# Performance work log

Hardware: AMD Instinct MI355X
Metric: run time of the kernel (lower is better)

The kernel has to match this reference:

```python
import jax, jax.numpy as jnp
import numpy as np

EPS = 1e-8


def setup_inputs() -> dict:
    key = jax.random.key(0)
    k1, k2, k3, k4 = jax.random.split(key, 4)
    B, N, M, C = 512, 512, 128, 1024
    addr = M + 6  # read head: k(M) + beta(1) + g(1) + s(3) + gamma(1)
    controller_out = jax.random.normal(k1, (B, C), dtype=jnp.float32)
    prev_w = jax.random.uniform(k2, (B, N), dtype=jnp.float32)
    prev_w = prev_w / prev_w.sum(axis=1, keepdims=True)  # valid weighting
    memory_state = jax.random.normal(k3, (B, N, M), dtype=jnp.float32)
    W_fc = jax.random.normal(k4, (C, addr), dtype=jnp.float32) * 0.02
    b_fc = jnp.zeros((addr,), dtype=jnp.float32)
    return {"controller_out": controller_out, "prev_w": prev_w,
            "memory_state": memory_state, "W_fc": W_fc, "b_fc": b_fc}


def reference(controller_out, prev_w, memory_state, W_fc, b_fc):
    M = memory_state.shape[2]
    out = controller_out @ W_fc + b_fc  # [B, M+6]
    k = out[:, :M]                                   # key
    beta = jax.nn.softplus(out[:, M:M + 1])          # key strength
    g = jax.nn.sigmoid(out[:, M + 1:M + 2])          # interpolation gate
    s = jax.nn.softmax(out[:, M + 2:M + 5], axis=1)  # 3-tap shift weights
    gamma = 1.0 + jax.nn.softplus(out[:, M + 5:M + 6])

    # Content addressing (Eq. 5-6): cosine similarity + sharpened softmax
    norm_k = jnp.linalg.norm(k, axis=1, keepdims=True) + EPS      # [B,1]
    norm_mem = jnp.linalg.norm(memory_state, axis=2) + EPS        # [B,N]
    sim = jnp.einsum('bnm,bm->bn', memory_state, k) / (norm_k * norm_mem)
    w_c = jax.nn.softmax(beta * sim, axis=1)

    # Interpolation (Eq. 7)
    w_g = g * w_c + (1.0 - g) * prev_w

    # Circular 3-tap shift (Eq. 8): vectorized roll instead of per-slot loop
    w_s = (s[:, 0:1] * jnp.roll(w_g, 1, axis=1)
           + s[:, 1:2] * w_g
           + s[:, 2:3] * jnp.roll(w_g, -1, axis=1))

    # Sharpening (Eq. 9)
    w_pow = w_s ** gamma
    w = w_pow / (w_pow.sum(axis=1, keepdims=True) + EPS)

    # Read vector (read head)
    read_vec = jnp.einsum('bn,bnm->bm', w, memory_state)
    return (read_vec, w)
```

## Files before the change

### kernel.cpp

```cpp
#include <hip/hip_runtime.h>
#include <math.h>

#define BB   512
#define NN   512
#define MM   128
#define CC   1024
#define ADDR 134
#define EPSF 1e-8f

#define KEEP(x) asm volatile("" : "+v"(x))

__device__ __forceinline__ float softplus_f(float x) {
    return fmaxf(x, 0.0f) + log1pf(expf(-fabsf(x)));
}

__global__ __launch_bounds__(1024, 4) void ntm_head_kernel(
    const float* __restrict__ co,
    const float* __restrict__ prev_w,
    const float* __restrict__ mem,
    const float* __restrict__ W_fc,
    const float* __restrict__ b_fc,
    float* __restrict__ out_rv,
    float* __restrict__ out_w)
{
    __shared__ __align__(16) float s_co[CC];
    __shared__ __align__(16) float s_k[MM];
    __shared__ float s_extra[8];
    __shared__ __align__(16) float s_bsim[NN];
    __shared__ float s_wg[NN];
    __shared__ float s_w[NN];
    __shared__ __align__(16) float s_part[32 * MM];
    __shared__ float s_red[16];
    __shared__ float s_params[8];

    const int t = threadIdx.x;
    const int b = blockIdx.x;
    const int gi = t >> 5;
    const int l  = t & 31;
    const float4* memb = (const float4*)(mem + (size_t)b * NN * MM);

    s_co[t] = co[(size_t)b * CC + t];
    float pw = (t < NN) ? prev_w[(size_t)b * NN + t] : 0.0f;

    float4 p[16];
    #pragma unroll
    for (int jj = 0; jj < 16; ++jj)
        p[jj] = memb[(size_t)gi * 32 + l + (size_t)jj * 1024];

    __syncthreads();

    {
        const int o    = t & (MM - 1);
        const int part = t >> 7;
        const float* Wp = W_fc + o;
        float a0 = 0.f, a1 = 0.f, a2 = 0.f, a3 = 0.f;
        const int c0 = part * (CC / 8);
        for (int c = c0; c < c0 + CC / 8; c += 4) {
            float4 cv = *(const float4*)(s_co + c);
            a0 = fmaf(cv.x, Wp[(size_t)(c + 0) * ADDR], a0);
            a1 = fmaf(cv.y, Wp[(size_t)(c + 1) * ADDR], a1);
            a2 = fmaf(cv.z, Wp[(size_t)(c + 2) * ADDR], a2);
            a3 = fmaf(cv.w, Wp[(size_t)(c + 3) * ADDR], a3);
        }
        s_part[part * MM + o] = (a0 + a1) + (a2 + a3);

        const int wv = t >> 6;
        if (wv < 6) {
            const int ll = t & 63;
            const int oe = MM + wv;
            const float* We = W_fc + oe;
            float e = 0.f;
            for (int c = ll; c < CC; c += 64)
                e = fmaf(s_co[c], We[(size_t)c * ADDR], e);
            #pragma unroll
            for (int off = 32; off >= 1; off >>= 1) e += __shfl_xor(e, off, 64);
            if (ll == 0) s_extra[wv] = e + b_fc[oe];
        }
    }

    #pragma unroll
    for (int jj = 0; jj < 16; ++jj) {
        KEEP(p[jj].x); KEEP(p[jj].y); KEEP(p[jj].z); KEEP(p[jj].w);
    }

    __syncthreads();

    if (t < MM) {
        float r = b_fc[t];
        #pragma unroll
        for (int q = 0; q < 8; ++q) r += s_part[q * MM + t];
        s_k[t] = r;
        float v = r * r;
        #pragma unroll
        for (int off = 32; off >= 1; off >>= 1) v += __shfl_xor(v, off, 64);
        if ((t & 63) == 0) s_red[t >> 6] = v;
    }
    __syncthreads();
    if (t == 0) {
        float ks = s_red[0] + s_red[1];
        float norm_k = sqrtf(ks) + EPSF;
        float beta = softplus_f(s_extra[0]);
        float g = 1.0f / (1.0f + expf(-s_extra[1]));
        float e0 = s_extra[2], e1 = s_extra[3], e2 = s_extra[4];
        float mx = fmaxf(e0, fmaxf(e1, e2));
        float x0 = expf(e0 - mx), x1 = expf(e1 - mx), x2 = expf(e2 - mx);
        float inv = 1.0f / (x0 + x1 + x2);
        s_params[0] = beta / norm_k;
        s_params[1] = g;
        s_params[2] = x0 * inv;
        s_params[3] = x1 * inv;
        s_params[4] = x2 * inv;
        s_params[5] = 1.0f + softplus_f(s_extra[5]);
    }
    __syncthreads();

    const float bnk = s_params[0];
    const float4 kv = ((const float4*)s_k)[l];

    #pragma unroll
    for (int j = 0; j < 16; j += 4) {
        float d0 = p[j  ].x*kv.x + p[j  ].y*kv.y + p[j  ].z*kv.z + p[j  ].w*kv.w;
        float d1 = p[j+1].x*kv.x + p[j+1].y*kv.y + p[j+1].z*kv.z + p[j+1].w*kv.w;
        float d2 = p[j+2].x*kv.x + p[j+2].y*kv.y + p[j+2].z*kv.z + p[j+2].w*kv.w;
        float d3 = p[j+3].x*kv.x + p[j+3].y*kv.y + p[j+3].z*kv.z + p[j+3].w*kv.w;
        float q0 = p[j  ].x*p[j  ].x + p[j  ].y*p[j  ].y + p[j  ].z*p[j  ].z + p[j  ].w*p[j  ].w;
        float q1 = p[j+1].x*p[j+1].x + p[j+1].y*p[j+1].y + p[j+1].z*p[j+1].z + p[j+1].w*p[j+1].w;
        float q2 = p[j+2].x*p[j+2].x + p[j+2].y*p[j+2].y + p[j+2].z*p[j+2].z + p[j+2].w*p[j+2].w;
        float q3 = p[j+3].x*p[j+3].x + p[j+3].y*p[j+3].y + p[j+3].z*p[j+3].z + p[j+3].w*p[j+3].w;

        d0 += __shfl_xor(d0, 16, 64); q0 += __shfl_xor(q0, 16, 64);
        d1 += __shfl_xor(d1, 16, 64); q1 += __shfl_xor(q1, 16, 64);
        d2 += __shfl_xor(d2, 16, 64); q2 += __shfl_xor(q2, 16, 64);
        d3 += __shfl_xor(d3, 16, 64); q3 += __shfl_xor(q3, 16, 64);
        float W0 = (l & 16) ? q0 : d0;
        float W1 = (l & 16) ? q1 : d1;
        float W2 = (l & 16) ? q2 : d2;
        float W3 = (l & 16) ? q3 : d3;
        W0 += __shfl_xor(W0, 8, 64); W1 += __shfl_xor(W1, 8, 64);
        W2 += __shfl_xor(W2, 8, 64); W3 += __shfl_xor(W3, 8, 64);
        float X0 = (l & 8) ? W1 : W0;
        float X1 = (l & 8) ? W3 : W2;
        X0 += __shfl_xor(X0, 4, 64); X1 += __shfl_xor(X1, 4, 64);
        float Y = (l & 4) ? X1 : X0;
        Y += __shfl_xor(Y, 2, 64);
        Y += __shfl_xor(Y, 1, 64);
        float Q = __shfl_xor(Y, 16, 64);
        if (l < 16 && (l & 3) == 0) {
            int jj = j + ((l & 4) >> 1) + ((l & 8) >> 3);
            s_bsim[gi + jj * 32] = bnk * Y / (sqrtf(Q) + EPSF);
        }
    }
    __syncthreads();

    float wp1 = 0.0f;
    {
        const float NEG = -3.0e38f;
        float b1 = (t < NN) ? s_bsim[t] : NEG;

        float m = b1;
        #pragma unroll
        for (int off = 32; off >= 1; off >>= 1) m = fmaxf(m, __shfl_xor(m, off, 64));
        if ((t & 63) == 0) s_red[t >> 6] = m;
        __syncthreads();
        float M8 = s_red[0];
        #pragma unroll
        for (int i = 1; i < 8; ++i) M8 = fmaxf(M8, s_red[i]);
        __syncthreads();

        float e1 = (t < NN) ? expf(b1 - M8) : 0.0f;
        float ls = e1;
        #pragma unroll
        for (int off = 32; off >= 1; off >>= 1) ls += __shfl_xor(ls, off, 64);
        if ((t & 63) == 0) s_red[t >> 6] = ls;
        __syncthreads();
        float S = s_red[0];
        #pragma unroll
        for (int i = 1; i < 8; ++i) S += s_red[i];
        __syncthreads();

        const float invS = 1.0f / S;
        const float g = s_params[1];
        float wg1 = fmaf(g, e1 * invS, (1.0f - g) * pw);
        if (t < NN) s_wg[t] = wg1;
        __syncthreads();

        const float sh0 = s_params[2], sh1 = s_params[3], sh2 = s_params[4];
        const float gamma = s_params[5];
        if (t < NN) {
            float ws1 = sh0 * s_wg[(t + NN - 1) & (NN - 1)]
                      + sh1 * wg1
                      + sh2 * s_wg[(t + 1) & (NN - 1)];
            wp1 = powf(ws1, gamma);
            s_w[t] = wp1;
        }
    }
    __syncthreads();

    {
        float4 acc = make_float4(0.f, 0.f, 0.f, 0.f);
        #pragma unroll
        for (int jj = 0; jj < 16; ++jj) {
            float w = s_w[gi + jj * 32];
            acc.x = fmaf(w, p[jj].x, acc.x);
            acc.y = fmaf(w, p[jj].y, acc.y);
            acc.z = fmaf(w, p[jj].z, acc.z);
            acc.w = fmaf(w, p[jj].w, acc.w);
        }

        float lz = wp1;
        #pragma unroll
        for (int off = 32; off >= 1; off >>= 1) lz += __shfl_xor(lz, off, 64);
        if ((t & 63) == 0) s_red[t >> 6] = lz;

        *((float4*)&s_part[gi * MM + l * 4]) = acc;
        __syncthreads();

        float Z = s_red[0];
        #pragma unroll
        for (int i = 1; i < 8; ++i) Z += s_red[i];
        const float invZ = 1.0f / (Z + EPSF);

        if (t < NN) out_w[(size_t)b * NN + t] = wp1 * invZ;

        if (t < 512) {
            const int h = t >> 7;
            const int o = t & (MM - 1);
            float r = 0.f;
            #pragma unroll
            for (int q = 0; q < 8; ++q) r += s_part[(h * 8 + q) * MM + o];
            s_bsim[h * MM + o] = r;
        }
        __syncthreads();
        if (t < MM) {
            float r = s_bsim[t] + s_bsim[MM + t] + s_bsim[2 * MM + t] + s_bsim[3 * MM + t];
            out_rv[(size_t)b * MM + t] = r * invZ;
        }
    }
}

extern "C" void kernel_launch(void* const* d_in, const int* in_sizes, int n_in,
                              void* d_out, int out_size, void* d_ws, size_t ws_size,
                              hipStream_t stream) {
    const float* co     = (const float*)d_in[0];
    const float* prev_w = (const float*)d_in[1];
    const float* mem    = (const float*)d_in[2];
    const float* W_fc   = (const float*)d_in[3];
    const float* b_fc   = (const float*)d_in[4];
    float* out = (float*)d_out;
    ntm_head_kernel<<<BB, 1024, 0, stream>>>(co, prev_w, mem, W_fc, b_fc,
                                             out, out + (size_t)BB * MM);
}
```

Before: 230.9 us.

## Split fused NTM head kernel into FC, similarity, and tail kernels

Replaces the single fused kernel, which held each batch's memory slice in registers, with three kernels. The first computes the FC projection for two batches per block so each W_fc load is shared, then writes the key scaled by beta/norm and the addressing parameters to workspace. The second spreads the cosine-similarity pass over four times as many smaller blocks. The third does the softmax, shift and sharpening and re-reads memory for the read vector. The aim is better parallelism and less register pressure, at the cost of reading the 134 MB memory tensor twice and adding launch and workspace traffic.

```diff
diff --git a/kernel.cpp b/kernel.cpp
--- a/kernel.cpp
+++ b/kernel.cpp
@@ -8,45 +8,31 @@
 #define ADDR 134
 #define EPSF 1e-8f
 
-#define KEEP(x) asm volatile("" : "+v"(x))
-
 __device__ __forceinline__ float softplus_f(float x) {
     return fmaxf(x, 0.0f) + log1pf(expf(-fabsf(x)));
 }
 
-__global__ __launch_bounds__(1024, 4) void ntm_head_kernel(
-    const float* __restrict__ co,
-    const float* __restrict__ prev_w,
-    const float* __restrict__ mem,
-    const float* __restrict__ W_fc,
-    const float* __restrict__ b_fc,
-    float* __restrict__ out_rv,
-    float* __restrict__ out_w)
+__global__ __launch_bounds__(512) void k1_fc(
+    const float* __restrict__ co, const float* __restrict__ W_fc,
+    const float* __restrict__ b_fc, float* __restrict__ ws_kk,
+    float* __restrict__ ws_par)
 {
-    __shared__ __align__(16) float s_co[CC];
-    __shared__ __align__(16) float s_k[MM];
-    __shared__ float s_extra[8];
-    __shared__ __align__(16) float s_bsim[NN];
-    __shared__ float s_wg[NN];
-    __shared__ float s_w[NN];
-    __shared__ __align__(16) float s_part[32 * MM];
-    __shared__ float s_red[16];
-    __shared__ float s_params[8];
-
-    const int t = threadIdx.x;
-    const int b = blockIdx.x;
-    const int gi = t >> 5;
-    const int l  = t & 31;
-    const float4* memb = (const float4*)(mem + (size_t)b * NN * MM);
-
-    s_co[t] = co[(size_t)b * CC + t];
-    float pw = (t < NN) ? prev_w[(size_t)b * NN + t] : 0.0f;
-
-    float4 p[16];
-    #pragma unroll
-    for (int jj = 0; jj < 16; ++jj)
-        p[jj] = memb[(size_t)gi * 32 + l + (size_t)jj * 1024];
-
+    __shared__ __align__(16) float s_co0[CC];
+    __shared__ __align__(16) float s_co1[CC];
+    __shared__ float s_part0[4 * MM];
+    __shared__ float s_part1[4 * MM];
+    __shared__ float s_extra[2][8];
+    __shared__ float s_red[2][2];
+    __shared__ float s_scale[2];
+
+    const int t  = threadIdx.x;
+    const int b0 = blockIdx.x;
+    const int b1 = blockIdx.x + 256;
+
+    s_co0[t]       = co[(size_t)b0 * CC + t];
+    s_co0[t + 512] = co[(size_t)b0 * CC + t + 512];
+    s_co1[t]       = co[(size_t)b1 * CC + t];
+    s_co1[t + 512] = co[(size_t)b1 * CC + t + 512];
     __syncthreads();
 
     {
@@ -54,79 +40,114 @@
         const int part = t >> 7;
         const float* Wp = W_fc + o;
         float a0 = 0.f, a1 = 0.f, a2 = 0.f, a3 = 0.f;
-        const int c0 = part * (CC / 8);
-        for (int c = c0; c < c0 + CC / 8; c += 4) {
-            float4 cv = *(const float4*)(s_co + c);
-            a0 = fmaf(cv.x, Wp[(size_t)(c + 0) * ADDR], a0);
-            a1 = fmaf(cv.y, Wp[(size_t)(c + 1) * ADDR], a1);
-            a2 = fmaf(cv.z, Wp[(size_t)(c + 2) * ADDR], a2);
-            a3 = fmaf(cv.w, Wp[(size_t)(c + 3) * ADDR], a3);
+        float d0 = 0.f, d1 = 0.f, d2 = 0.f, d3 = 0.f;
+        const int cc0 = part * 256;
+        for (int c = cc0; c < cc0 + 256; c += 4) {
+            float w0 = Wp[(size_t)(c + 0) * ADDR];
+            float w1 = Wp[(size_t)(c + 1) * ADDR];
+            float w2 = Wp[(size_t)(c + 2) * ADDR];
+            float w3 = Wp[(size_t)(c + 3) * ADDR];
+            float4 u = *(const float4*)(s_co0 + c);
+            float4 v = *(const float4*)(s_co1 + c);
+            a0 = fmaf(u.x, w0, a0); a1 = fmaf(u.y, w1, a1);
+            a2 = fmaf(u.z, w2, a2); a3 = fmaf(u.w, w3, a3);
+            d0 = fmaf(v.x, w0, d0); d1 = fmaf(v.y, w1, d1);
+            d2 = fmaf(v.z, w2, d2); d3 = fmaf(v.w, w3, d3);
         }
-        s_part[part * MM + o] = (a0 + a1) + (a2 + a3);
+        s_part0[part * MM + o] = (a0 + a1) + (a2 + a3);
+        s_part1[part * MM + o] = (d0 + d1) + (d2 + d3);
 
         const int wv = t >> 6;
         if (wv < 6) {
             const int ll = t & 63;
             const int oe = MM + wv;
             const float* We = W_fc + oe;
-            float e = 0.f;
-            for (int c = ll; c < CC; c += 64)
-                e = fmaf(s_co[c], We[(size_t)c * ADDR], e);
+            float e0 = 0.f, e1 = 0.f;
+            for (int c = ll; c < CC; c += 64) {
+                float w = We[(size_t)c * ADDR];
+                e0 = fmaf(s_co0[c], w, e0);
+                e1 = fmaf(s_co1[c], w, e1);
+            }
             #pragma unroll
-            for (int off = 32; off >= 1; off >>= 1) e += __shfl_xor(e, off, 64);
-            if (ll == 0) s_extra[wv] = e + b_fc[oe];
+            for (int off = 32; off >= 1; off >>= 1) {
+                e0 += __shfl_xor(e0, off, 64);
+                e1 += __shfl_xor(e1, off, 64);
+            }
+            if (ll == 0) {
+                s_extra[0][wv] = e0 + b_fc[oe];
+                s_extra[1][wv] = e1 + b_fc[oe];
+            }
         }
     }
-
-    #pragma unroll
-    for (int jj = 0; jj < 16; ++jj) {
-        KEEP(p[jj].x); KEEP(p[jj].y); KEEP(p[jj].z); KEEP(p[jj].w);
-    }
-
-    __syncthreads();
-
+    __syncthreads();
+
+    float k0 = 0.f, k1v = 0.f;
     if (t < MM) {
-        float r = b_fc[t];
+        float bias = b_fc[t];
+        k0  = bias + s_part0[t] + s_part0[MM + t] + s_part0[2 * MM + t] + s_part0[3 * MM + t];
+        k1v = bias + s_part1[t] + s_part1[MM + t] + s_part1[2 * MM + t] + s_part1[3 * MM + t];
+        float v0 = k0 * k0, v1 = k1v * k1v;
         #pragma unroll
-        for (int q = 0; q < 8; ++q) r += s_part[q * MM + t];
-        s_k[t] = r;
-        float v = r * r;
-        #pragma unroll
-        for (int off = 32; off >= 1; off >>= 1) v += __shfl_xor(v, off, 64);
-        if ((t & 63) == 0) s_red[t >> 6] = v;
-    }
-    __syncthreads();
-    if (t == 0) {
-        float ks = s_red[0] + s_red[1];
+        for (int off = 32; off >= 1; off >>= 1) {
+            v0 += __shfl_xor(v0, off, 64);
+            v1 += __shfl_xor(v1, off, 64);
+        }
+        if ((t & 63) == 0) { s_red[0][t >> 6] = v0; s_red[1][t >> 6] = v1; }
+    }
+    __syncthreads();
+    if (t < 2) {
+        const int bs = t;
+        const int bb = bs ? b1 : b0;
+        float ks = s_red[bs][0] + s_red[bs][1];
         float norm_k = sqrtf(ks) + EPSF;
-        float beta = softplus_f(s_extra[0]);
-        float g = 1.0f / (1.0f + expf(-s_extra[1]));
-        float e0 = s_extra[2], e1 = s_extra[3], e2 = s_extra[4];
+        float beta = softplus_f(s_extra[bs][0]);
+        float g = 1.0f / (1.0f + expf(-s_extra[bs][1]));
+        float e0 = s_extra[bs][2], e1 = s_extra[bs][3], e2 = s_extra[bs][4];
         float mx = fmaxf(e0, fmaxf(e1, e2));
         float x0 = expf(e0 - mx), x1 = expf(e1 - mx), x2 = expf(e2 - mx);
         float inv = 1.0f / (x0 + x1 + x2);
-        s_params[0] = beta / norm_k;
-        s_params[1] = g;
-        s_params[2] = x0 * inv;
-        s_params[3] = x1 * inv;
-        s_params[4] = x2 * inv;
-        s_params[5] = 1.0f + softplus_f(s_extra[5]);
-    }
-    __syncthreads();
-
-    const float bnk = s_params[0];
-    const float4 kv = ((const float4*)s_k)[l];
+        s_scale[bs] = beta / norm_k;
+        float* pp = ws_par + (size_t)bb * 8;
+        pp[0] = g;
+        pp[1] = x0 * inv; pp[2] = x1 * inv; pp[3] = x2 * inv;
+        pp[4] = 1.0f + softplus_f(s_extra[bs][5]);
+    }
+    __syncthreads();
+    if (t < MM) {
+        ws_kk[(size_t)b0 * MM + t] = k0  * s_scale[0];
+        ws_kk[(size_t)b1 * MM + t] = k1v * s_scale[1];
+    }
+}
+
+__global__ __launch_bounds__(256) void k2_sim(
+    const float* __restrict__ mem, const float* __restrict__ ws_kk,
+    float* __restrict__ ws_bsim)
+{
+    const int bb   = blockIdx.x;
+    const int b    = bb >> 2;
+    const int tile = bb & 3;
+    const int t = threadIdx.x;
+    const int g = t >> 5;
+    const int l = t & 31;
+    const float4* memb = (const float4*)(mem + (size_t)b * NN * MM) + (size_t)tile * 128 * 32;
+    const float4 kv = ((const float4*)(ws_kk + (size_t)b * MM))[l];
+    float* bs = ws_bsim + (size_t)b * NN + tile * 128;
 
     #pragma unroll
     for (int j = 0; j < 16; j += 4) {
-        float d0 = p[j  ].x*kv.x + p[j  ].y*kv.y + p[j  ].z*kv.z + p[j  ].w*kv.w;
-        float d1 = p[j+1].x*kv.x + p[j+1].y*kv.y + p[j+1].z*kv.z + p[j+1].w*kv.w;
-        float d2 = p[j+2].x*kv.x + p[j+2].y*kv.y + p[j+2].z*kv.z + p[j+2].w*kv.w;
-        float d3 = p[j+3].x*kv.x + p[j+3].y*kv.y + p[j+3].z*kv.z + p[j+3].w*kv.w;
-        float q0 = p[j  ].x*p[j  ].x + p[j  ].y*p[j  ].y + p[j  ].z*p[j  ].z + p[j  ].w*p[j  ].w;
-        float q1 = p[j+1].x*p[j+1].x + p[j+1].y*p[j+1].y + p[j+1].z*p[j+1].z + p[j+1].w*p[j+1].w;
-        float q2 = p[j+2].x*p[j+2].x + p[j+2].y*p[j+2].y + p[j+2].z*p[j+2].z + p[j+2].w*p[j+2].w;
-        float q3 = p[j+3].x*p[j+3].x + p[j+3].y*p[j+3].y + p[j+3].z*p[j+3].z + p[j+3].w*p[j+3].w;
+        float4 a0 = memb[(size_t)(g + (j + 0) * 8) * 32 + l];
+        float4 a1 = memb[(size_t)(g + (j + 1) * 8) * 32 + l];
+        float4 a2 = memb[(size_t)(g + (j + 2) * 8) * 32 + l];
+        float4 a3 = memb[(size_t)(g + (j + 3) * 8) * 32 + l];
+
+        float d0 = a0.x*kv.x + a0.y*kv.y + a0.z*kv.z + a0.w*kv.w;
+        float d1 = a1.x*kv.x + a1.y*kv.y + a1.z*kv.z + a1.w*kv.w;
+        float d2 = a2.x*kv.x + a2.y*kv.y + a2.z*kv.z + a2.w*kv.w;
+        float d3 = a3.x*kv.x + a3.y*kv.y + a3.z*kv.z + a3.w*kv.w;
+        float q0 = a0.x*a0.x + a0.y*a0.y + a0.z*a0.z + a0.w*a0.w;
+        float q1 = a1.x*a1.x + a1.y*a1.y + a1.z*a1.z + a1.w*a1.w;
+        float q2 = a2.x*a2.x + a2.y*a2.y + a2.z*a2.z + a2.w*a2.w;
+        float q3 = a3.x*a3.x + a3.y*a3.y + a3.z*a3.z + a3.w*a3.w;
 
         d0 += __shfl_xor(d0, 16, 64); q0 += __shfl_xor(q0, 16, 64);
         d1 += __shfl_xor(d1, 16, 64); q1 += __shfl_xor(q1, 16, 64);
@@ -147,94 +168,120 @@
         float Q = __shfl_xor(Y, 16, 64);
         if (l < 16 && (l & 3) == 0) {
             int jj = j + ((l & 4) >> 1) + ((l & 8) >> 3);
-            s_bsim[gi + jj * 32] = bnk * Y / (sqrtf(Q) + EPSF);
+            bs[g + jj * 8] = Y / (sqrtf(Q) + EPSF);
         }
     }
+}
+
+__global__ __launch_bounds__(1024) void k3_tail(
+    const float* __restrict__ prev_w, const float* __restrict__ mem,
+    const float* __restrict__ ws_bsim, const float* __restrict__ ws_par,
+    float* __restrict__ out_rv, float* __restrict__ out_w)
+{
+    __shared__ float s_wg[NN];
+    __shared__ float s_w[NN];
+    __shared__ __align__(16) float s_part[32 * MM];
+    __shared__ float s_scr[4 * MM];
+    __shared__ float s_red[16];
+
+    const int t = threadIdx.x;
+    const int b = blockIdx.x;
+    const int gi = t >> 5;
+    const int l  = t & 31;
+    const float4* memb = (const float4*)(mem + (size_t)b * NN * MM);
+
+    float pw = (t < NN) ? prev_w[(size_t)b * NN + t] : 0.0f;
+    const float NEG = -3.0e38f;
+    float b1 = (t < NN) ? ws_bsim[(size_t)b * NN + t] : NEG;
+    const float g     = ws_par[(size_t)b * 8 + 0];
+    const float sh0   = ws_par[(size_t)b * 8 + 1];
+    const float sh1   = ws_par[(size_t)b * 8 + 2];
+    const float sh2   = ws_par[(size_t)b * 8 + 3];
+    const float gamma = ws_par[(size_t)b * 8 + 4];
+
+    float m = b1;
+    #pragma unroll
+    for (int off = 32; off >= 1; off >>= 1) m = fmaxf(m, __shfl_xor(m, off, 64));
+    if ((t & 63) == 0) s_red[t >> 6] = m;
+    __syncthreads();
+    float M8 = s_red[0];
+    #pragma unroll
+    for (int i = 1; i < 8; ++i) M8 = fmaxf(M8, s_red[i]);
+    __syncthreads();
+
+    float e1 = (t < NN) ? expf(b1 - M8) : 0.0f;
+    float ls = e1;
+    #pragma unroll
+    for (int off = 32; off >= 1; off >>= 1) ls += __shfl_xor(ls, off, 64);
+    if ((t & 63) == 0) s_red[t >> 6] = ls;
+    __syncthreads();
+    float S = s_red[0];
+    #pragma unroll
+    for (int i = 1; i < 8; ++i) S += s_red[i];
+    __syncthreads();
+
+    const float invS = 1.0f / S;
+    float wg1 = fmaf(g, e1 * invS, (1.0f - g) * pw);
+    if (t < NN) s_wg[t] = wg1;
     __syncthreads();
 
     float wp1 = 0.0f;
-    {
-        const float NEG = -3.0e38f;
-        float b1 = (t < NN) ? s_bsim[t] : NEG;
-
-        float m = b1;
+    if (t < NN) {
+        float ws1 = sh0 * s_wg[(t + NN - 1) & (NN - 1)]
+                  + sh1 * wg1
+                  + sh2 * s_wg[(t + 1) & (NN - 1)];
+        wp1 = powf(ws1, gamma);
+        s_w[t] = wp1;
+    }
+    __syncthreads();
+
+    float4 acc = make_float4(0.f, 0.f, 0.f, 0.f);
+    for (int j = 0; j < 16; j += 4) {
+        float4 a0 = memb[(size_t)(gi + (j + 0) * 32) * 32 + l];
+        float4 a1 = memb[(size_t)(gi + (j + 1) * 32) * 32 + l];
+        float4 a2 = memb[(size_t)(gi + (j + 2) * 32) * 32 + l];
+        float4 a3 = memb[(size_t)(gi + (j + 3) * 32) * 32 + l];
+        float w0 = s_w[gi + (j + 0) * 32];
+        float w1 = s_w[gi + (j + 1) * 32];
+        float w2 = s_w[gi + (j + 2) * 32];
+        float w3 = s_w[gi + (j + 3) * 32];
+        acc.x = fmaf(w0, a0.x, acc.x); acc.y = fmaf(w0, a0.y, acc.y);
+        acc.z = fmaf(w0, a0.z, acc.z); acc.w = fmaf(w0, a0.w, acc.w);
+        acc.x = fmaf(w1, a1.x, acc.x); acc.y = fmaf(w1, a1.y, acc.y);
+        acc.z = fmaf(w1, a1.z, acc.z); acc.w = fmaf(w1, a1.w, acc.w);
+        acc.x = fmaf(w2, a2.x, acc.x); acc.y = fmaf(w2, a2.y, acc.y);
+        acc.z = fmaf(w2, a2.z, acc.z); acc.w = fmaf(w2, a2.w, acc.w);
+        acc.x = fmaf(w3, a3.x, acc.x); acc.y = fmaf(w3, a3.y, acc.y);
+        acc.z = fmaf(w3, a3.z, acc.z); acc.w = fmaf(w3, a3.w, acc.w);
+    }
+
+    float lz = wp1;
+    #pragma unroll
+    for (int off = 32; off >= 1; off >>= 1) lz += __shfl_xor(lz, off, 64);
+    if ((t & 63) == 0) s_red[t >> 6] = lz;
+
+    *((float4*)&s_part[gi * MM + l * 4]) = acc;
+    __syncthreads();
+
+    float Z = s_red[0];
+    #pragma unroll
+    for (int i = 1; i < 8; ++i) Z += s_red[i];
+    const float invZ = 1.0f / (Z + EPSF);
+
+    if (t < NN) out_w[(size_t)b * NN + t] = wp1 * invZ;
+
+    if (t < 512) {
+        const int h = t >> 7;
+        const int o = t & (MM - 1);
+        float r = 0.f;
         #pragma unroll
-        for (int off = 32; off >= 1; off >>= 1) m = fmaxf(m, __shfl_xor(m, off, 64));
-        if ((t & 63) == 0) s_red[t >> 6] = m;
-        __syncthreads();
-        float M8 = s_red[0];
-        #pragma unroll
-        for (int i = 1; i < 8; ++i) M8 = fmaxf(M8, s_red[i]);
-        __syncthreads();
-
-        float e1 = (t < NN) ? expf(b1 - M8) : 0.0f;
-        float ls = e1;
-        #pragma unroll
-        for (int off = 32; off >= 1; off >>= 1) ls += __shfl_xor(ls, off, 64);
-        if ((t & 63) == 0) s_red[t >> 6] = ls;
-        __syncthreads();
-        float S = s_red[0];
-        #pragma unroll
-        for (int i = 1; i < 8; ++i) S += s_red[i];
-        __syncthreads();
-
-        const float invS = 1.0f / S;
-        const float g = s_params[1];
-        float wg1 = fmaf(g, e1 * invS, (1.0f - g) * pw);
-        if (t < NN) s_wg[t] = wg1;
-        __syncthreads();
-
-        const float sh0 = s_params[2], sh1 = s_params[3], sh2 = s_params[4];
-        const float gamma = s_params[5];
-        if (t < NN) {
-            float ws1 = sh0 * s_wg[(t + NN - 1) & (NN - 1)]
-                      + sh1 * wg1
-                      + sh2 * s_wg[(t + 1) & (NN - 1)];
-            wp1 = powf(ws1, gamma);
-            s_w[t] = wp1;
-        }
-    }
-    __syncthreads();
-
-    {
-        float4 acc = make_float4(0.f, 0.f, 0.f, 0.f);
-        #pragma unroll
-        for (int jj = 0; jj < 16; ++jj) {
-            float w = s_w[gi + jj * 32];
-            acc.x = fmaf(w, p[jj].x, acc.x);
-            acc.y = fmaf(w, p[jj].y, acc.y);
-            acc.z = fmaf(w, p[jj].z, acc.z);
-            acc.w = fmaf(w, p[jj].w, acc.w);
-        }
-
-        float lz = wp1;
-        #pragma unroll
-        for (int off = 32; off >= 1; off >>= 1) lz += __shfl_xor(lz, off, 64);
-        if ((t & 63) == 0) s_red[t >> 6] = lz;
-
-        *((float4*)&s_part[gi * MM + l * 4]) = acc;
-        __syncthreads();
-
-        float Z = s_red[0];
-        #pragma unroll
-        for (int i = 1; i < 8; ++i) Z += s_red[i];
-        const float invZ = 1.0f / (Z + EPSF);
-
-        if (t < NN) out_w[(size_t)b * NN + t] = wp1 * invZ;
-
-        if (t < 512) {
-            const int h = t >> 7;
-            const int o = t & (MM - 1);
-            float r = 0.f;
-            #pragma unroll
-            for (int q = 0; q < 8; ++q) r += s_part[(h * 8 + q) * MM + o];
-            s_bsim[h * MM + o] = r;
-        }
-        __syncthreads();
-        if (t < MM) {
-            float r = s_bsim[t] + s_bsim[MM + t] + s_bsim[2 * MM + t] + s_bsim[3 * MM + t];
-            out_rv[(size_t)b * MM + t] = r * invZ;
-        }
+        for (int q = 0; q < 8; ++q) r += s_part[(h * 8 + q) * MM + o];
+        s_scr[h * MM + o] = r;
+    }
+    __syncthreads();
+    if (t < MM) {
+        float r = s_scr[t] + s_scr[MM + t] + s_scr[2 * MM + t] + s_scr[3 * MM + t];
+        out_rv[(size_t)b * MM + t] = r * invZ;
     }
 }
 
@@ -247,6 +294,14 @@
     const float* W_fc   = (const float*)d_in[3];
     const float* b_fc   = (const float*)d_in[4];
     float* out = (float*)d_out;
-    ntm_head_kernel<<<BB, 1024, 0, stream>>>(co, prev_w, mem, W_fc, b_fc,
-                                             out, out + (size_t)BB * MM);
-}
+
+    float* ws      = (float*)d_ws;
+    float* ws_kk   = ws;
+    float* ws_par  = ws + 65536;
+    float* ws_bsim = ws + 65536 + 4096;
+
+    k1_fc  <<<256,  512, 0, stream>>>(co, W_fc, b_fc, ws_kk, ws_par);
+    k2_sim <<<2048, 256, 0, stream>>>(mem, ws_kk, ws_bsim);
+    k3_tail<<<512, 1024, 0, stream>>>(prev_w, mem, ws_bsim, ws_par,
+                                      out, out + (size_t)BB * MM);
+}
```

Result: slower. 251.0 us (+8.7%).

## Drop register-resident memory tile and re-stream rows from global per phase

Applied to the files above, without the earlier changes.

Removes the 16 float4 per-thread register cache of the memory tile that was prefetched before the FC matvec. Instead, memory rows are loaded from global separately in the similarity pass and again in the read pass. The launch-bounds occupancy hint rises from 4 to 8. This aims to cut register pressure and allow more resident waves. In exchange, the per-block memory tile is read twice and the prefetch that overlapped the FC stage is lost. It also swaps expf and powf for the fast __expf/__logf intrinsics and moves the Z reduction ahead of the barrier.

```diff
diff --git a/kernel.cpp b/kernel.cpp
--- a/kernel.cpp
+++ b/kernel.cpp
@@ -8,13 +8,11 @@
 #define ADDR 134
 #define EPSF 1e-8f
 
-#define KEEP(x) asm volatile("" : "+v"(x))
-
 __device__ __forceinline__ float softplus_f(float x) {
     return fmaxf(x, 0.0f) + log1pf(expf(-fabsf(x)));
 }
 
-__global__ __launch_bounds__(1024, 4) void ntm_head_kernel(
+__global__ __launch_bounds__(1024, 8) void ntm_head_kernel(
     const float* __restrict__ co,
     const float* __restrict__ prev_w,
     const float* __restrict__ mem,
@@ -41,12 +39,6 @@
 
     s_co[t] = co[(size_t)b * CC + t];
     float pw = (t < NN) ? prev_w[(size_t)b * NN + t] : 0.0f;
-
-    float4 p[16];
-    #pragma unroll
-    for (int jj = 0; jj < 16; ++jj)
-        p[jj] = memb[(size_t)gi * 32 + l + (size_t)jj * 1024];
-
     __syncthreads();
 
     {
@@ -77,18 +69,12 @@
             if (ll == 0) s_extra[wv] = e + b_fc[oe];
         }
     }
-
-    #pragma unroll
-    for (int jj = 0; jj < 16; ++jj) {
-        KEEP(p[jj].x); KEEP(p[jj].y); KEEP(p[jj].z); KEEP(p[jj].w);
-    }
-
     __syncthreads();
 
     if (t < MM) {
         float r = b_fc[t];
         #pragma unroll
-        for (int q = 0; q < 8; ++q) r += s_part[q * MM + t];
+        for (int p = 0; p < 8; ++p) r += s_part[p * MM + t];
         s_k[t] = r;
         float v = r * r;
         #pragma unroll
@@ -100,10 +86,10 @@
         float ks = s_red[0] + s_red[1];
         float norm_k = sqrtf(ks) + EPSF;
         float beta = softplus_f(s_extra[0]);
-        float g = 1.0f / (1.0f + expf(-s_extra[1]));
+        float g = 1.0f / (1.0f + __expf(-s_extra[1]));
         float e0 = s_extra[2], e1 = s_extra[3], e2 = s_extra[4];
         float mx = fmaxf(e0, fmaxf(e1, e2));
-        float x0 = expf(e0 - mx), x1 = expf(e1 - mx), x2 = expf(e2 - mx);
+        float x0 = __expf(e0 - mx), x1 = __expf(e1 - mx), x2 = __expf(e2 - mx);
         float inv = 1.0f / (x0 + x1 + x2);
         s_params[0] = beta / norm_k;
         s_params[1] = g;
@@ -119,14 +105,19 @@
 
     #pragma unroll
     for (int j = 0; j < 16; j += 4) {
-        float d0 = p[j  ].x*kv.x + p[j  ].y*kv.y + p[j  ].z*kv.z + p[j  ].w*kv.w;
-        float d1 = p[j+1].x*kv.x + p[j+1].y*kv.y + p[j+1].z*kv.z + p[j+1].w*kv.w;
-        float d2 = p[j+2].x*kv.x + p[j+2].y*kv.y + p[j+2].z*kv.z + p[j+2].w*kv.w;
-        float d3 = p[j+3].x*kv.x + p[j+3].y*kv.y + p[j+3].z*kv.z + p[j+3].w*kv.w;
-        float q0 = p[j  ].x*p[j  ].x + p[j  ].y*p[j  ].y + p[j  ].z*p[j  ].z + p[j  ].w*p[j  ].w;
-        float q1 = p[j+1].x*p[j+1].x + p[j+1].y*p[j+1].y + p[j+1].z*p[j+1].z + p[j+1].w*p[j+1].w;
-        float q2 = p[j+2].x*p[j+2].x + p[j+2].y*p[j+2].y + p[j+2].z*p[j+2].z + p[j+2].w*p[j+2].w;
-        float q3 = p[j+3].x*p[j+3].x + p[j+3].y*p[j+3].y + p[j+3].z*p[j+3].z + p[j+3].w*p[j+3].w;
+        float4 a0 = memb[(size_t)(gi + (j + 0) * 32) * 32 + l];
+        float4 a1 = memb[(size_t)(gi + (j + 1) * 32) * 32 + l];
+        float4 a2 = memb[(size_t)(gi + (j + 2) * 32) * 32 + l];
+        float4 a3 = memb[(size_t)(gi + (j + 3) * 32) * 32 + l];
+
+        float d0 = a0.x*kv.x + a0.y*kv.y + a0.z*kv.z + a0.w*kv.w;
+        float q0 = a0.x*a0.x + a0.y*a0.y + a0.z*a0.z + a0.w*a0.w;
+        float d1 = a1.x*kv.x + a1.y*kv.y + a1.z*kv.z + a1.w*kv.w;
+        float q1 = a1.x*a1.x + a1.y*a1.y + a1.z*a1.z + a1.w*a1.w;
+        float d2 = a2.x*kv.x + a2.y*kv.y + a2.z*kv.z + a2.w*kv.w;
+        float q2 = a2.x*a2.x + a2.y*a2.y + a2.z*a2.z + a2.w*a2.w;
+        float d3 = a3.x*kv.x + a3.y*kv.y + a3.z*kv.z + a3.w*kv.w;
+        float q3 = a3.x*a3.x + a3.y*a3.y + a3.z*a3.z + a3.w*a3.w;
 
         d0 += __shfl_xor(d0, 16, 64); q0 += __shfl_xor(q0, 16, 64);
         d1 += __shfl_xor(d1, 16, 64); q1 += __shfl_xor(q1, 16, 64);
@@ -167,7 +158,7 @@
         for (int i = 1; i < 8; ++i) M8 = fmaxf(M8, s_red[i]);
         __syncthreads();
 
-        float e1 = (t < NN) ? expf(b1 - M8) : 0.0f;
+        float e1 = (t < NN) ? __expf(b1 - M8) : 0.0f;
         float ls = e1;
         #pragma unroll
         for (int off = 32; off >= 1; off >>= 1) ls += __shfl_xor(ls, off, 64);
@@ -190,30 +181,38 @@
             float ws1 = sh0 * s_wg[(t + NN - 1) & (NN - 1)]
                       + sh1 * wg1
                       + sh2 * s_wg[(t + 1) & (NN - 1)];
-            wp1 = powf(ws1, gamma);
+            wp1 = __expf(gamma * __logf(fmaxf(ws1, 1e-37f)));
             s_w[t] = wp1;
         }
     }
+
+    float lz = wp1;
+    #pragma unroll
+    for (int off = 32; off >= 1; off >>= 1) lz += __shfl_xor(lz, off, 64);
+    if ((t & 63) == 0) s_red[t >> 6] = lz;
     __syncthreads();
 
     {
         float4 acc = make_float4(0.f, 0.f, 0.f, 0.f);
-        #pragma unroll
-        for (int jj = 0; jj < 16; ++jj) {
-            float w = s_w[gi + jj * 32];
-            acc.x = fmaf(w, p[jj].x, acc.x);
-            acc.y = fmaf(w, p[jj].y, acc.y);
-            acc.z = fmaf(w, p[jj].z, acc.z);
-            acc.w = fmaf(w, p[jj].w, acc.w);
-        }
-
-        float lz = wp1;
-        #pragma unroll
-        for (int off = 32; off >= 1; off >>= 1) lz += __shfl_xor(lz, off, 64);
-        if ((t & 63) == 0) s_red[t >> 6] = lz;
-
+        for (int j = 0; j < 16; j += 4) {
+            float4 a0 = memb[(size_t)(gi + (j + 0) * 32) * 32 + l];
+            float4 a1 = memb[(size_t)(gi + (j + 1) * 32) * 32 + l];
+            float4 a2 = memb[(size_t)(gi + (j + 2) * 32) * 32 + l];
+            float4 a3 = memb[(size_t)(gi + (j + 3) * 32) * 32 + l];
+            float w0 = s_w[gi + (j + 0) * 32];
+            float w1 = s_w[gi + (j + 1) * 32];
+            float w2 = s_w[gi + (j + 2) * 32];
+            float w3 = s_w[gi + (j + 3) * 32];
+            acc.x = fmaf(w0, a0.x, acc.x); acc.y = fmaf(w0, a0.y, acc.y);
+            acc.z = fmaf(w0, a0.z, acc.z); acc.w = fmaf(w0, a0.w, acc.w);
+            acc.x = fmaf(w1, a1.x, acc.x); acc.y = fmaf(w1, a1.y, acc.y);
+            acc.z = fmaf(w1, a1.z, acc.z); acc.w = fmaf(w1, a1.w, acc.w);
+            acc.x = fmaf(w2, a2.x, acc.x); acc.y = fmaf(w2, a2.y, acc.y);
+            acc.z = fmaf(w2, a2.z, acc.z); acc.w = fmaf(w2, a2.w, acc.w);
+            acc.x = fmaf(w3, a3.x, acc.x); acc.y = fmaf(w3, a3.y, acc.y);
+            acc.z = fmaf(w3, a3.z, acc.z); acc.w = fmaf(w3, a3.w, acc.w);
+        }
         *((float4*)&s_part[gi * MM + l * 4]) = acc;
-        __syncthreads();
 
         float Z = s_red[0];
         #pragma unroll
@@ -221,6 +220,7 @@
         const float invZ = 1.0f / (Z + EPSF);
 
         if (t < NN) out_w[(size_t)b * NN + t] = wp1 * invZ;
+        __syncthreads();
 
         if (t < 512) {
             const int h = t >> 7;
```

Measured after the change: 227.6 us. No clear change (-1.4%).
